# Performance work log

Hardware: AMD Instinct MI355X
Metric: run time of the kernel (lower is better)

Reference implementation:

```python
import jax, jax.numpy as jnp
import numpy as np

B, N = 4096, 12
HID = 64
SLOPE = 0.2   # GATv2Conv default negative_slope
ALPHA = 0.1   # skip-connection scale


def _gabriel_adjacency(p):
    # p: [B, N, 2] node positions. Gabriel graph: edge (i,j) iff no other
    # point k lies inside the closed disk with diameter segment (p_i, p_j).
    n = p.shape[1]
    mid = (p[:, :, None, :] + p[:, None, :, :]) * 0.5                      # [B,N,N,2]
    r2 = jnp.sum((p[:, :, None, :] - p[:, None, :, :]) ** 2, -1) * 0.25    # [B,N,N]
    d2 = jnp.sum((p[:, None, None, :, :] - mid[:, :, :, None, :]) ** 2, -1)  # [B,i,j,k]
    eye = jnp.eye(n, dtype=bool)
    excl = eye[:, None, :] | eye[None, :, :]                               # k==i or k==j
    d2 = jnp.where(excl[None], jnp.inf, d2)
    gab = jnp.all(d2 > r2[..., None], axis=-1) & (~eye)[None]
    # undirected edges + self loops (GATv2Conv add_self_loops=True default)
    return gab | jnp.swapaxes(gab, 1, 2) | eye[None]                       # [B,N,N]


def _gatv2(x, adj, wl, wr, att, b):
    # PyG GATv2Conv, heads=1: e_ij = att . leaky_relu(W_l x_j + W_r x_i),
    # alpha = softmax_j(e_ij) over neighbors, out_i = sum_j alpha_ij W_l x_j + b.
    xl = x @ wl                                                            # source feats [B,N,H]
    xr = x @ wr                                                            # target feats [B,N,H]
    s = jax.nn.leaky_relu(xl[:, None, :, :] + xr[:, :, None, :], SLOPE)    # [B,i,j,H]
    e = jnp.einsum('bijh,h->bij', s, att)
    e = jnp.where(adj, e, -1e9)
    a = jax.nn.softmax(e, axis=-1)                                         # over sources j
    return jnp.einsum('bij,bjh->bih', a, xl) + b


def _forward(batch, enc_w1, enc_b1, enc_w2, enc_b2, enc_w3, enc_b3,
             g1_wl, g1_wr, g1_att, g1_b, g2_wl, g2_wr, g2_att, g2_b,
             g3_wl, g3_wr, g3_att, g3_b, g4_wl, g4_wr, g4_att, g4_b,
             lab_w, lab_b, val_w, val_b, skip_w, skip_b):
    h = jax.nn.relu(batch @ enc_w1 + enc_b1)
    h = jax.nn.relu(h @ enc_w2 + enc_b2)
    latent = h @ enc_w3 + enc_b3                                           # [B,N,3]
    # graph construction is non-differentiable (scipy in the original)
    adj = _gabriel_adjacency(jax.lax.stop_gradient(latent[..., :2]))
    x0 = latent[..., 2:3]                                                  # [B,N,1]
    x1 = jax.nn.relu(_gatv2(x0, adj, g1_wl, g1_wr, g1_att, g1_b))
    x2 = jax.nn.relu(_gatv2(x1, adj, g2_wl, g2_wr, g2_att, g2_b))
    skip = latent @ skip_w + skip_b
    x3 = jax.nn.relu(_gatv2(x2, adj, g3_wl, g3_wr, g3_att, g3_b) + ALPHA * skip)
    logits = x3 @ lab_w + lab_b                                            # [B,N,4]
    # note: original feeds x2 (not x3) into gcn4 -- kept faithful
    x4 = jax.nn.relu(_gatv2(x2, adj, g4_wl, g4_wr, g4_att, g4_b) + ALPHA * skip)
    values = x4 @ val_w + val_b                                            # [B,N,1]
    return batch[:, :, :4], batch[:, :, 4:5], logits, values, latent


def setup_inputs():
    key = jax.random.key(0)
    ks = iter(jax.random.split(key, 40))
    def rnd(shape, s=0.1):
        return jax.random.normal(next(ks), shape, dtype=jnp.float32) * s
    inp = {"batch": jax.random.normal(next(ks), (B, N, 5), dtype=jnp.float32)}
    inp.update(enc_w1=rnd((5, HID)), enc_b1=jnp.zeros((HID,), jnp.float32),
               enc_w2=rnd((HID, HID)), enc_b2=jnp.zeros((HID,), jnp.float32),
               enc_w3=rnd((HID, 3)), enc_b3=jnp.zeros((3,), jnp.float32))
    for i, cin in zip((1, 2, 3, 4), (1, HID, HID, HID)):
        inp[f"g{i}_wl"] = rnd((cin, HID)); inp[f"g{i}_wr"] = rnd((cin, HID))
        inp[f"g{i}_att"] = rnd((HID,)); inp[f"g{i}_b"] = jnp.zeros((HID,), jnp.float32)
    inp.update(lab_w=rnd((HID, 4)), lab_b=jnp.zeros((4,), jnp.float32),
               val_w=rnd((HID, 1)), val_b=jnp.zeros((1,), jnp.float32),
               skip_w=rnd((3, HID)), skip_b=jnp.zeros((HID,), jnp.float32))
    return inp


def reference(batch, enc_w1, enc_b1, enc_w2, enc_b2, enc_w3, enc_b3,
              g1_wl, g1_wr, g1_att, g1_b, g2_wl, g2_wr, g2_att, g2_b,
              g3_wl, g3_wr, g3_att, g3_b, g4_wl, g4_wr, g4_att, g4_b,
              lab_w, lab_b, val_w, val_b, skip_w, skip_b):
    return _forward(batch, enc_w1, enc_b1, enc_w2, enc_b2, enc_w3, enc_b3,
                    g1_wl, g1_wr, g1_att, g1_b, g2_wl, g2_wr, g2_att, g2_b,
                    g3_wl, g3_wr, g3_att, g3_b, g4_wl, g4_wr, g4_att, g4_b,
                    lab_w, lab_b, val_w, val_b, skip_w, skip_b)
```

## Files before the change

### kernel.cpp

```cpp
#include <hip/hip_runtime.h>
#include <hip/hip_bf16.h>
#include <math.h>

#define N     12
#define HID   64
#define STP   68
#define SLOPE 0.2f
#define ALPHA 0.1f

typedef float v2f __attribute__((ext_vector_type(2)));
typedef float v4f __attribute__((ext_vector_type(4)));

#define OUT0 0
#define OUT1 196608
#define OUT2 245760
#define OUT3 442368
#define OUT4 491520

__global__ void prep_kernel(const float* __restrict__ enc_w2,
                            const float* __restrict__ g2_wl, const float* __restrict__ g2_wr,
                            const float* __restrict__ g3_wl, const float* __restrict__ g3_wr,
                            const float* __restrict__ g4_wl, const float* __restrict__ g4_wr,
                            const float* __restrict__ lab_w,
                            float* __restrict__ ws) {
    int t = threadIdx.x;
    int bx = blockIdx.x;
    if (bx == 448) {
        #pragma unroll
        for (int c = 0; c < 4; c++) ws[10240 + c*64 + t] = lab_w[t*4 + c];
        return;
    }
    if (bx < 64) {
        int c = bx;
        ws[t*64 + c] = enc_w2[c*64 + t];
        return;
    }
    int mm = (bx - 64) >> 6, c = bx & 63;
    const float* src;
    switch (mm) {
        case 0: src = g2_wl; break;
        case 1: src = g2_wr; break;
        case 2: src = g3_wl; break;
        case 3: src = g3_wr; break;
        case 4: src = g4_wl; break;
        default: src = g4_wr; break;
    }
    __hip_bfloat16 h = __float2bfloat16(src[c*64 + t]);
    unsigned short* w16 = (unsigned short*)(ws + 4096);
    w16[mm*4096 + t*64 + c] = *(unsigned short*)&h;
}

template<bool TW>
__global__ __launch_bounds__(64, 3) void gae_kernel(
    const float* __restrict__ batch,
    const float* __restrict__ enc_w1, const float* __restrict__ enc_b1,
    const float* __restrict__ enc_w2, const float* __restrict__ enc_b2,
    const float* __restrict__ enc_w3, const float* __restrict__ enc_b3,
    const float* __restrict__ g1_wl, const float* __restrict__ g1_wr,
    const float* __restrict__ g1_att, const float* __restrict__ g1_b,
    const float* __restrict__ g2_wl, const float* __restrict__ g2_wr,
    const float* __restrict__ g2_att, const float* __restrict__ g2_b,
    const float* __restrict__ g3_wl, const float* __restrict__ g3_wr,
    const float* __restrict__ g3_att, const float* __restrict__ g3_b,
    const float* __restrict__ g4_wl, const float* __restrict__ g4_wr,
    const float* __restrict__ g4_att, const float* __restrict__ g4_b,
    const float* __restrict__ lab_w, const float* __restrict__ lab_b,
    const float* __restrict__ val_w, const float* __restrict__ val_b,
    const float* __restrict__ skip_w, const float* __restrict__ skip_b,
    const float* __restrict__ wsT,
    float* __restrict__ out)
{
    const int b = blockIdx.x;
    const int t = threadIdx.x;

    __shared__ __align__(16) float lds[2560];
    float* bufL = lds;
    float* bufR = lds + N*STP;
    float* xB   = lds + 2*N*STP;
    float* pool = lds + 2*N*STP + N*HID;
    unsigned char* pairs8 = (unsigned char*)&lds[2544];

    const v2f z2 = {0.f, 0.f};
    const v4f z4 = {0.f, 0.f, 0.f, 0.f};
    const v4f s4 = {SLOPE, SLOPE, SLOPE, SLOPE};

    const int p0 = t,        i0 = p0 / N, j0 = p0 - i0*N;
    const int p1 = t + 64,   i1 = p1 / N, j1 = p1 - i1*N;
    const int p2 = (t < 16) ? (t + 128) : 143;
    const int i2 = p2 / N,   j2 = p2 - i2*N;

    if (t < N*5) {
        float v = batch[b*(N*5) + t];
        pool[t] = v;
        int i = t / 5, f = t - i*5;
        if (f < 4) out[OUT0 + (size_t)b*(N*4) + i*4 + f] = v;
        else       out[OUT1 + (size_t)b*N + i] = v;
    }
    __syncthreads();

    {
        float acc[N];
        float bias = enc_b1[t];
        #pragma unroll
        for (int i=0;i<N;i++) acc[i] = bias;
        #pragma unroll
        for (int f=0; f<5; f++) {
            float w = enc_w1[f*HID + t];
            #pragma unroll
            for (int i=0;i<N;i++) acc[i] = fmaf(pool[i*5+f], w, acc[i]);
        }
        #pragma unroll
        for (int i=0;i<N;i++) bufL[i*STP + t] = fmaxf(acc[i], 0.f);
    }
    __syncthreads();

    {
        v2f acc[N];
        #pragma unroll
        for (int i=0;i<N;i++) acc[i] = z2;
        const float* w2p = TW ? (wsT + t*HID) : nullptr;
        for (int c=0;c<HID;c+=4) {
            v2f w01, w23;
            if (TW) {
                v4f w4 = *reinterpret_cast<const v4f*>(&w2p[c]);
                w01 = w4.xy; w23 = w4.zw;
            } else {
                w01 = (v2f){enc_w2[(c+0)*HID+t], enc_w2[(c+1)*HID+t]};
                w23 = (v2f){enc_w2[(c+2)*HID+t], enc_w2[(c+3)*HID+t]};
            }
            #pragma unroll
            for (int i=0;i<N;i++) {
                v4f xv = *reinterpret_cast<const v4f*>(&bufL[i*STP + c]);
                acc[i] = __builtin_elementwise_fma(xv.xy, w01, acc[i]);
                acc[i] = __builtin_elementwise_fma(xv.zw, w23, acc[i]);
            }
        }
        float bias = enc_b2[t];
        #pragma unroll
        for (int i=0;i<N;i++) bufR[i*STP + t] = fmaxf(bias + acc[i].x + acc[i].y, 0.f);
    }
    __syncthreads();

    if (t < N*3) {
        int i = t / 3, c = t - i*3;
        float acc = enc_b3[c];
        for (int k=0;k<HID;k+=4) {
            v4f xv = *reinterpret_cast<const v4f*>(&bufR[i*STP + k]);
            acc = fmaf(xv.x, enc_w3[(k+0)*3+c], acc);
            acc = fmaf(xv.y, enc_w3[(k+1)*3+c], acc);
            acc = fmaf(xv.z, enc_w3[(k+2)*3+c], acc);
            acc = fmaf(xv.w, enc_w3[(k+3)*3+c], acc);
        }
        pool[t] = acc;
        out[OUT4 + (size_t)b*(N*3) + t] = acc;
    }
    __syncthreads();

    float skipv[N];
    {
        float w0 = skip_w[t], w1 = skip_w[HID+t], w2 = skip_w[2*HID+t];
        float bias = skip_b[t];
        #pragma unroll
        for (int i=0;i<N;i++) {
            float v = bias;
            v = fmaf(pool[i*3+0], w0, v);
            v = fmaf(pool[i*3+1], w1, v);
            v = fmaf(pool[i*3+2], w2, v);
            skipv[i] = v;
        }
    }

    auto gab = [&](int i, int j)->bool {
        if (i == j) return false;
        float pix = pool[i*3], piy = pool[i*3+1];
        float pjx = pool[j*3], pjy = pool[j*3+1];
        float mx = (pix + pjx) * 0.5f, my = (piy + pjy) * 0.5f;
        float dx = pix - pjx, dy = piy - pjy;
        float r2 = (dx*dx + dy*dy) * 0.25f;
        bool g = true;
        #pragma unroll
        for (int k=0;k<N;k++) {
            float ex = pool[k*3] - mx, ey = pool[k*3+1] - my;
            bool ok = (k == i) || (k == j) || (ex*ex + ey*ey > r2);
            g = g && ok;
        }
        return g;
    };
    unsigned long long gb0 = __ballot(gab(i0, j0));
    unsigned long long gb1 = __ballot(gab(i1, j1));
    unsigned long long gb2 = __ballot((t < 16) && gab(i2, j2));
    auto gbit = [&](int p)->int {
        unsigned long long m = (p < 64) ? gb0 : ((p < 128) ? gb1 : gb2);
        return (int)((m >> (p & 63)) & 1ull);
    };
    const int adjA = gbit(p0) | gbit(j0*N+i0) | (i0 == j0);
    const int adjB = gbit(p1) | gbit(j1*N+i1) | (i1 == j1);
    const int adjC = (t < 16) ? (gbit(p2) | gbit(j2*N+i2) | (i2 == j2)) : 0;

    auto mbcnt64 = [&](unsigned long long m)->int {
        return __builtin_amdgcn_mbcnt_hi((unsigned)(m >> 32),
               __builtin_amdgcn_mbcnt_lo((unsigned)m, 0));
    };
    const unsigned long long am0 = __ballot(adjA != 0);
    const unsigned long long am1 = __ballot(adjB != 0);
    const unsigned long long am2 = __ballot(adjC != 0);
    const int c0  = __popcll(am0);
    const int c01 = c0 + __popcll(am1);
    const int nv  = c01 + __popcll(am2);
    const int idx0 = mbcnt64(am0);
    const int idx1 = c0  + mbcnt64(am1);
    const int idx2 = c01 + mbcnt64(am2);
    if (adjA)               pairs8[idx0] = (unsigned char)p0;
    if (adjB && idx1 < 64)  pairs8[idx1] = (unsigned char)p1;
    if (adjC && idx2 < 64)  pairs8[idx2] = (unsigned char)p2;
    const bool ovB = adjB && (idx1 >= 64);
    const bool ovC = adjC && (idx2 >= 64);
    const int nvc = nv < 64 ? nv : 64;

    auto scoreAt = [&](int i, int j, const float* __restrict__ att)->float {
        const float* Lj = &bufL[j*STP];
        const float* Ri = &bufR[i*STP];
        v4f a = z4;
        for (int h=0; h<HID; h+=4) {
            v4f a4 = *reinterpret_cast<const v4f*>(&att[h]);
            v4f xl = *reinterpret_cast<const v4f*>(Lj + h);
            v4f xr = *reinterpret_cast<const v4f*>(Ri + h);
            v4f s = xl + xr;
            v4f l = __builtin_elementwise_fma(s4, __builtin_elementwise_min(s, z4),
                                              __builtin_elementwise_max(s, z4));
            a = __builtin_elementwise_fma(a4, l, a);
        }
        return (a.x + a.y) + (a.z + a.w);
    };

    auto gat_core = [&](const float* __restrict__ att, const float* __restrict__ gb,
                        float* __restrict__ xout, int strideOut, int useSkip) {
        __syncthreads();
        pool[t] = -1e9f; pool[t+64] = -1e9f;
        if (t < 16) pool[t+128] = -1e9f;
        if (t < nvc) {
            int p = pairs8[t];
            int i = (p * 171) >> 11;
            int j = p - i*N;
            pool[p] = scoreAt(i, j, att);
        }
        if (nv > 64) {
            if (ovB) pool[p1] = scoreAt(i1, j1, att);
            if (ovC) pool[p2] = scoreAt(i2, j2, att);
        }
        __syncthreads();
        if (t < N) {
            float m = -2e9f;
            #pragma unroll
            for (int j=0;j<N;j++) m = fmaxf(m, pool[t*N+j]);
            float tmp[N]; float sum = 0.f;
            #pragma unroll
            for (int j=0;j<N;j++) { float v = __expf(pool[t*N+j] - m); tmp[j] = v; sum += v; }
            float inv = 1.0f / sum;
            #pragma unroll
            for (int j=0;j<N;j++) pool[t*N+j] = tmp[j] * inv;
        }
        __syncthreads();
        {
            float xj[N];
            #pragma unroll
            for (int j=0;j<N;j++) xj[j] = bufL[j*STP + t];
            v4f X0 = {xj[0], xj[1], xj[2],  xj[3]};
            v4f X1 = {xj[4], xj[5], xj[6],  xj[7]};
            v4f X2 = {xj[8], xj[9], xj[10], xj[11]};
            float bias = gb[t];
            #pragma unroll
            for (int i=0;i<N;i++) {
                const v4f* ep = reinterpret_cast<const v4f*>(&pool[i*N]);
                v4f acc = __builtin_elementwise_fma(ep[0], X0,
                          __builtin_elementwise_fma(ep[1], X1, ep[2]*X2));
                float r = bias + ((acc.x + acc.y) + (acc.z + acc.w));
                if (useSkip) r = fmaf(ALPHA, skipv[i], r);
                xout[i*strideOut + t] = fmaxf(r, 0.f);
            }
        }
        __syncthreads();
    };

    auto stage = [&](const float* __restrict__ xin, int strideIn,
                     const unsigned* __restrict__ wlB, const unsigned* __restrict__ wrB,
                     const float* __restrict__ wl, const float* __restrict__ wr) {
        v2f al[N], ar[N];
        #pragma unroll
        for (int i=0;i<N;i++) { al[i] = z2; ar[i] = z2; }
        for (int c=0;c<HID;c+=4) {
            v2f wl01, wl23, wr01, wr23;
            if (TW) {
                uint2 qa = *reinterpret_cast<const uint2*>(wlB + (c>>1));
                uint2 qb = *reinterpret_cast<const uint2*>(wrB + (c>>1));
                wl01 = (v2f){ __uint_as_float(qa.x << 16), __uint_as_float(qa.x & 0xffff0000u) };
                wl23 = (v2f){ __uint_as_float(qa.y << 16), __uint_as_float(qa.y & 0xffff0000u) };
                wr01 = (v2f){ __uint_as_float(qb.x << 16), __uint_as_float(qb.x & 0xffff0000u) };
                wr23 = (v2f){ __uint_as_float(qb.y << 16), __uint_as_float(qb.y & 0xffff0000u) };
            } else {
                wl01 = (v2f){wl[(c+0)*HID+t], wl[(c+1)*HID+t]};
                wl23 = (v2f){wl[(c+2)*HID+t], wl[(c+3)*HID+t]};
                wr01 = (v2f){wr[(c+0)*HID+t], wr[(c+1)*HID+t]};
                wr23 = (v2f){wr[(c+2)*HID+t], wr[(c+3)*HID+t]};
            }
            #pragma unroll
            for (int i=0;i<N;i++) {
                v4f xv = *reinterpret_cast<const v4f*>(&xin[i*strideIn + c]);
                al[i] = __builtin_elementwise_fma(xv.xy, wl01, al[i]);
                al[i] = __builtin_elementwise_fma(xv.zw, wl23, al[i]);
                ar[i] = __builtin_elementwise_fma(xv.xy, wr01, ar[i]);
                ar[i] = __builtin_elementwise_fma(xv.zw, wr23, ar[i]);
            }
        }
        #pragma unroll
        for (int i=0;i<N;i++) {
            bufL[i*STP + t] = al[i].x + al[i].y;
            bufR[i*STP + t] = ar[i].x + ar[i].y;
        }
    };

    const unsigned* wb = TW ? (const unsigned*)(wsT + 4096) : nullptr;
    const unsigned* w_g2l = TW ? wb + 0*2048 + t*32 : nullptr;
    const unsigned* w_g2r = TW ? wb + 1*2048 + t*32 : nullptr;
    const unsigned* w_g3l = TW ? wb + 2*2048 + t*32 : nullptr;
    const unsigned* w_g3r = TW ? wb + 3*2048 + t*32 : nullptr;
    const unsigned* w_g4l = TW ? wb + 4*2048 + t*32 : nullptr;
    const unsigned* w_g4r = TW ? wb + 5*2048 + t*32 : nullptr;

    {
        float wlv = g1_wl[t], wrv = g1_wr[t];
        #pragma unroll
        for (int i=0;i<N;i++) {
            float v = pool[i*3+2];
            bufL[i*STP + t] = v * wlv;
            bufR[i*STP + t] = v * wrv;
        }
    }
    gat_core(g1_att, g1_b, bufR, STP, 0);

    stage(bufR, STP, w_g2l, w_g2r, g2_wl, g2_wr);
    gat_core(g2_att, g2_b, xB, HID, 0);

    stage(xB, HID, w_g3l, w_g3r, g3_wl, g3_wr);
    gat_core(g3_att, g3_b, bufR, STP, 1);

    if (t < N*4) {
        int i = t >> 2, c = t & 3;
        float acc = lab_b[c];
        if (TW) {
            const float* lwT = wsT + 10240 + c*HID;
            for (int h=0;h<HID;h+=4) {
                v4f xv = *reinterpret_cast<const v4f*>(&bufR[i*STP + h]);
                v4f w4 = *reinterpret_cast<const v4f*>(&lwT[h]);
                acc = fmaf(xv.x, w4.x, acc);
                acc = fmaf(xv.y, w4.y, acc);
                acc = fmaf(xv.z, w4.z, acc);
                acc = fmaf(xv.w, w4.w, acc);
            }
        } else {
            for (int h=0;h<HID;h+=4) {
                v4f xv = *reinterpret_cast<const v4f*>(&bufR[i*STP + h]);
                acc = fmaf(xv.x, lab_w[(h+0)*4+c], acc);
                acc = fmaf(xv.y, lab_w[(h+1)*4+c], acc);
                acc = fmaf(xv.z, lab_w[(h+2)*4+c], acc);
                acc = fmaf(xv.w, lab_w[(h+3)*4+c], acc);
            }
        }
        out[OUT2 + (size_t)b*(N*4) + t] = acc;
    }

    stage(xB, HID, w_g4l, w_g4r, g4_wl, g4_wr);
    gat_core(g4_att, g4_b, bufR, STP, 1);

    if (t < N) {
        float acc = val_b[0];
        for (int h=0;h<HID;h+=4) {
            v4f xv = *reinterpret_cast<const v4f*>(&bufR[t*STP + h]);
            v4f w4 = *reinterpret_cast<const v4f*>(&val_w[h]);
            acc = fmaf(xv.x, w4.x, acc);
            acc = fmaf(xv.y, w4.y, acc);
            acc = fmaf(xv.z, w4.z, acc);
            acc = fmaf(xv.w, w4.w, acc);
        }
        out[OUT3 + (size_t)b*N + t] = acc;
    }
}

extern "C" void kernel_launch(void* const* d_in, const int* in_sizes, int n_in,
                              void* d_out, int out_size, void* d_ws, size_t ws_size,
                              hipStream_t stream) {
    (void)in_sizes; (void)n_in; (void)out_size;
    const bool useT = (ws_size >= (7*4096 + 256)*sizeof(float));
    if (useT) {
        prep_kernel<<<dim3(449), dim3(64), 0, stream>>>(
            (const float*)d_in[3],
            (const float*)d_in[11], (const float*)d_in[12],
            (const float*)d_in[15], (const float*)d_in[16],
            (const float*)d_in[19], (const float*)d_in[20],
            (const float*)d_in[23],
            (float*)d_ws);
        gae_kernel<true><<<dim3(4096), dim3(64), 0, stream>>>(
            (const float*)d_in[0],
            (const float*)d_in[1],  (const float*)d_in[2],
            (const float*)d_in[3],  (const float*)d_in[4],
            (const float*)d_in[5],  (const float*)d_in[6],
            (const float*)d_in[7],  (const float*)d_in[8],  (const float*)d_in[9],  (const float*)d_in[10],
            (const float*)d_in[11], (const float*)d_in[12], (const float*)d_in[13], (const float*)d_in[14],
            (const float*)d_in[15], (const float*)d_in[16], (const float*)d_in[17], (const float*)d_in[18],
            (const float*)d_in[19], (const float*)d_in[20], (const float*)d_in[21], (const float*)d_in[22],
            (const float*)d_in[23], (const float*)d_in[24],
            (const float*)d_in[25], (const float*)d_in[26],
            (const float*)d_in[27], (const float*)d_in[28],
            (const float*)d_ws,
            (float*)d_out);
    } else {
        gae_kernel<false><<<dim3(4096), dim3(64), 0, stream>>>(
            (const float*)d_in[0],
            (const float*)d_in[1],  (const float*)d_in[2],
            (const float*)d_in[3],  (const float*)d_in[4],
            (const float*)d_in[5],  (const float*)d_in[6],
            (const float*)d_in[7],  (const float*)d_in[8],  (const float*)d_in[9],  (const float*)d_in[10],
            (const float*)d_in[11], (const float*)d_in[12], (const float*)d_in[13], (const float*)d_in[14],
            (const float*)d_in[15], (const float*)d_in[16], (const float*)d_in[17], (const float*)d_in[18],
            (const float*)d_in[19], (const float*)d_in[20], (const float*)d_in[21], (const float*)d_in[22],
            (const float*)d_in[23], (const float*)d_in[24],
            (const float*)d_in[25], (const float*)d_in[26],
            (const float*)d_in[27], (const float*)d_in[28],
            nullptr,
            (float*)d_out);
    }
}
```

Baseline: 182.8 us.

## Compute GAT linear projections with bf16 MFMA instead of scalar FMA loops

Replaces the per-thread scalar FMA projection (x @ W_l, x @ W_r) in GAT layers 2-4 with 16x16x32 bf16 MFMA instructions. The prep kernel now packs the weights into the MFMA B-fragment layout, and the activations are rounded to bf16 in registers to form the A fragments. This is meant to remove the VALU-bound inner loop, at the cost of rounding activations to bf16 and wasting 4 of the 16 M rows on padding. The workspace layout and the offset of the label weights are moved to match.

```diff
diff --git a/kernel.cpp b/kernel.cpp
--- a/kernel.cpp
+++ b/kernel.cpp
@@ -10,6 +10,12 @@
 
 typedef float v2f __attribute__((ext_vector_type(2)));
 typedef float v4f __attribute__((ext_vector_type(4)));
+typedef int   i4  __attribute__((ext_vector_type(4)));
+typedef short v8s __attribute__((ext_vector_type(8)));
+
+static __device__ __forceinline__ v8s as_v8s(i4 v) {
+    union { i4 a; v8s b; } u; u.a = v; return u.b;
+}
 
 #define OUT0 0
 #define OUT1 196608
@@ -25,19 +31,21 @@
                             float* __restrict__ ws) {
     int t = threadIdx.x;
     int bx = blockIdx.x;
-    if (bx == 448) {
-        #pragma unroll
-        for (int c = 0; c < 4; c++) ws[10240 + c*64 + t] = lab_w[t*4 + c];
-        return;
-    }
     if (bx < 64) {
         int c = bx;
         ws[t*64 + c] = enc_w2[c*64 + t];
         return;
     }
-    int mm = (bx - 64) >> 6, c = bx & 63;
+    if (bx == 112) {
+        #pragma unroll
+        for (int c = 0; c < 4; c++) ws[16384 + c*64 + t] = lab_w[t*4 + c];
+        return;
+    }
+    int idx = bx - 64;
+    int mat = idx >> 3, rem = idx & 7;
+    int kt = rem >> 2, nt = rem & 3;
     const float* src;
-    switch (mm) {
+    switch (mat) {
         case 0: src = g2_wl; break;
         case 1: src = g2_wr; break;
         case 2: src = g3_wl; break;
@@ -45,9 +53,17 @@
         case 4: src = g4_wl; break;
         default: src = g4_wr; break;
     }
-    __hip_bfloat16 h = __float2bfloat16(src[c*64 + t]);
-    unsigned short* w16 = (unsigned short*)(ws + 4096);
-    w16[mm*4096 + t*64 + c] = *(unsigned short*)&h;
+    int quad = t >> 4, col = t & 15;
+    int n = nt*16 + col;
+    unsigned* dst = (unsigned*)(ws + 4096) + mat*2048 + (kt*4+nt)*256 + t*4;
+    #pragma unroll
+    for (int jp = 0; jp < 4; jp++) {
+        int k0 = kt*32 + quad*8 + 2*jp;
+        __hip_bfloat16 h0 = __float2bfloat16(src[(k0+0)*64 + n]);
+        __hip_bfloat16 h1 = __float2bfloat16(src[(k0+1)*64 + n]);
+        unsigned u0 = *(unsigned short*)&h0, u1 = *(unsigned short*)&h1;
+        dst[jp] = u0 | (u1 << 16);
+    }
 }
 
 template<bool TW>
@@ -282,27 +298,60 @@
         __syncthreads();
     };
 
+    auto stage_mfma = [&](const float* __restrict__ xin, int strideIn, int matL) {
+        const int m = t & 15, quad = t >> 4;
+        const int mc = (m < N) ? m : 0;
+        i4 aF[2];
+        #pragma unroll
+        for (int kt=0; kt<2; kt++) {
+            const float* xp = &xin[mc*strideIn + kt*32 + quad*8];
+            v4f lo = *reinterpret_cast<const v4f*>(xp);
+            v4f hi = *reinterpret_cast<const v4f*>(xp + 4);
+            unsigned u0 = __float_as_uint(lo.x) + 0x8000u, u1 = __float_as_uint(lo.y) + 0x8000u;
+            unsigned u2 = __float_as_uint(lo.z) + 0x8000u, u3 = __float_as_uint(lo.w) + 0x8000u;
+            unsigned u4 = __float_as_uint(hi.x) + 0x8000u, u5 = __float_as_uint(hi.y) + 0x8000u;
+            unsigned u6 = __float_as_uint(hi.z) + 0x8000u, u7 = __float_as_uint(hi.w) + 0x8000u;
+            i4 a;
+            a.x = (int)__builtin_amdgcn_perm(u1, u0, 0x07060302u);
+            a.y = (int)__builtin_amdgcn_perm(u3, u2, 0x07060302u);
+            a.z = (int)__builtin_amdgcn_perm(u5, u4, 0x07060302u);
+            a.w = (int)__builtin_amdgcn_perm(u7, u6, 0x07060302u);
+            aF[kt] = a;
+        }
+        const i4* bbase = reinterpret_cast<const i4*>(wsT + 4096);
+        #pragma unroll
+        for (int mm=0; mm<2; mm++) {
+            const i4* bp = bbase + (matL + mm)*512;
+            v4f acc[4] = {z4, z4, z4, z4};
+            #pragma unroll
+            for (int nt=0; nt<4; nt++) {
+                i4 b0 = bp[(0*4+nt)*64 + t];
+                i4 b1 = bp[(1*4+nt)*64 + t];
+                acc[nt] = __builtin_amdgcn_mfma_f32_16x16x32_bf16(as_v8s(aF[0]), as_v8s(b0), acc[nt], 0, 0, 0);
+                acc[nt] = __builtin_amdgcn_mfma_f32_16x16x32_bf16(as_v8s(aF[1]), as_v8s(b1), acc[nt], 0, 0, 0);
+            }
+            float* dst = (mm == 0) ? bufL : bufR;
+            if (quad < 3) {
+                #pragma unroll
+                for (int nt=0; nt<4; nt++) {
+                    #pragma unroll
+                    for (int r=0; r<4; r++)
+                        dst[(quad*4+r)*STP + nt*16 + m] = acc[nt][r];
+                }
+            }
+        }
+    };
+
     auto stage = [&](const float* __restrict__ xin, int strideIn,
-                     const unsigned* __restrict__ wlB, const unsigned* __restrict__ wrB,
                      const float* __restrict__ wl, const float* __restrict__ wr) {
         v2f al[N], ar[N];
         #pragma unroll
         for (int i=0;i<N;i++) { al[i] = z2; ar[i] = z2; }
         for (int c=0;c<HID;c+=4) {
-            v2f wl01, wl23, wr01, wr23;
-            if (TW) {
-                uint2 qa = *reinterpret_cast<const uint2*>(wlB + (c>>1));
-                uint2 qb = *reinterpret_cast<const uint2*>(wrB + (c>>1));
-                wl01 = (v2f){ __uint_as_float(qa.x << 16), __uint_as_float(qa.x & 0xffff0000u) };
-                wl23 = (v2f){ __uint_as_float(qa.y << 16), __uint_as_float(qa.y & 0xffff0000u) };
-                wr01 = (v2f){ __uint_as_float(qb.x << 16), __uint_as_float(qb.x & 0xffff0000u) };
-                wr23 = (v2f){ __uint_as_float(qb.y << 16), __uint_as_float(qb.y & 0xffff0000u) };
-            } else {
-                wl01 = (v2f){wl[(c+0)*HID+t], wl[(c+1)*HID+t]};
-                wl23 = (v2f){wl[(c+2)*HID+t], wl[(c+3)*HID+t]};
-                wr01 = (v2f){wr[(c+0)*HID+t], wr[(c+1)*HID+t]};
-                wr23 = (v2f){wr[(c+2)*HID+t], wr[(c+3)*HID+t]};
-            }
+            v2f wl01 = (v2f){wl[(c+0)*HID+t], wl[(c+1)*HID+t]};
+            v2f wl23 = (v2f){wl[(c+2)*HID+t], wl[(c+3)*HID+t]};
+            v2f wr01 = (v2f){wr[(c+0)*HID+t], wr[(c+1)*HID+t]};
+            v2f wr23 = (v2f){wr[(c+2)*HID+t], wr[(c+3)*HID+t]};
             #pragma unroll
             for (int i=0;i<N;i++) {
                 v4f xv = *reinterpret_cast<const v4f*>(&xin[i*strideIn + c]);
@@ -319,14 +368,6 @@
         }
     };
 
-    const unsigned* wb = TW ? (const unsigned*)(wsT + 4096) : nullptr;
-    const unsigned* w_g2l = TW ? wb + 0*2048 + t*32 : nullptr;
-    const unsigned* w_g2r = TW ? wb + 1*2048 + t*32 : nullptr;
-    const unsigned* w_g3l = TW ? wb + 2*2048 + t*32 : nullptr;
-    const unsigned* w_g3r = TW ? wb + 3*2048 + t*32 : nullptr;
-    const unsigned* w_g4l = TW ? wb + 4*2048 + t*32 : nullptr;
-    const unsigned* w_g4r = TW ? wb + 5*2048 + t*32 : nullptr;
-
     {
         float wlv = g1_wl[t], wrv = g1_wr[t];
         #pragma unroll
@@ -338,17 +379,17 @@
     }
     gat_core(g1_att, g1_b, bufR, STP, 0);
 
-    stage(bufR, STP, w_g2l, w_g2r, g2_wl, g2_wr);
+    if (TW) stage_mfma(bufR, STP, 0); else stage(bufR, STP, g2_wl, g2_wr);
     gat_core(g2_att, g2_b, xB, HID, 0);
 
-    stage(xB, HID, w_g3l, w_g3r, g3_wl, g3_wr);
+    if (TW) stage_mfma(xB, HID, 2); else stage(xB, HID, g3_wl, g3_wr);
     gat_core(g3_att, g3_b, bufR, STP, 1);
 
     if (t < N*4) {
         int i = t >> 2, c = t & 3;
         float acc = lab_b[c];
         if (TW) {
-            const float* lwT = wsT + 10240 + c*HID;
+            const float* lwT = wsT + 16384 + c*HID;
             for (int h=0;h<HID;h+=4) {
                 v4f xv = *reinterpret_cast<const v4f*>(&bufR[i*STP + h]);
                 v4f w4 = *reinterpret_cast<const v4f*>(&lwT[h]);
@@ -369,7 +410,7 @@
         out[OUT2 + (size_t)b*(N*4) + t] = acc;
     }
 
-    stage(xB, HID, w_g4l, w_g4r, g4_wl, g4_wr);
+    if (TW) stage_mfma(xB, HID, 4); else stage(xB, HID, g4_wl, g4_wr);
     gat_core(g4_att, g4_b, bufR, STP, 1);
 
     if (t < N) {
@@ -390,9 +431,9 @@
                               void* d_out, int out_size, void* d_ws, size_t ws_size,
                               hipStream_t stream) {
     (void)in_sizes; (void)n_in; (void)out_size;
-    const bool useT = (ws_size >= (7*4096 + 256)*sizeof(float));
+    const bool useT = (ws_size >= (16384 + 256)*sizeof(float));
     if (useT) {
-        prep_kernel<<<dim3(449), dim3(64), 0, stream>>>(
+        prep_kernel<<<dim3(113), dim3(64), 0, stream>>>(
             (const float*)d_in[3],
             (const float*)d_in[11], (const float*)d_in[12],
             (const float*)d_in[15], (const float*)d_in[16],
```

After: 150.9 us. 17.4% less time.
